# Kernel tuning notes

Measured on AMD Instinct MI355X. Metric: run time of the kernel, lower is better.

## Reference

```python
import jax, jax.numpy as jnp
import numpy as np

SEQ, BATCH, HID = 4096, 32, 512


def setup_inputs() -> dict:
    key = jax.random.key(0)
    ks = jax.random.split(key, 7)
    s = 1.0 / np.sqrt(HID)
    return {
        "x0": jax.random.normal(ks[0], (SEQ, BATCH, 1), dtype=jnp.float32),
        "W_ih": jax.random.uniform(ks[1], (4 * HID, 1), jnp.float32, -s, s),
        "W_hh": jax.random.uniform(ks[2], (4 * HID, HID), jnp.float32, -s, s),
        "b_ih": jax.random.uniform(ks[3], (4 * HID,), jnp.float32, -s, s),
        "b_hh": jax.random.uniform(ks[4], (4 * HID,), jnp.float32, -s, s),
        "W_lin": jax.random.uniform(ks[5], (1, HID), jnp.float32, -s, s),
        "b_lin": jax.random.uniform(ks[6], (1,), jnp.float32, -s, s),
    }


def _lstm(x0, W_ih, W_hh, b_ih, b_hh):
    # x0: (T, B, 1). Precompute input contribution to gates for all steps.
    x_proj = jnp.einsum("tbi,gi->tbg", x0, W_ih) + (b_ih + b_hh)  # (T, B, 4H)
    T, B, _ = x_proj.shape
    H = W_hh.shape[1]
    h0 = jnp.zeros((B, H), x0.dtype)
    c0 = jnp.zeros((B, H), x0.dtype)

    def step(carry, xp):
        h, c = carry
        gates = xp + h @ W_hh.T  # (B, 4H)
        i, f, g, o = jnp.split(gates, 4, axis=-1)  # torch gate order i,f,g,o
        i = jax.nn.sigmoid(i)
        f = jax.nn.sigmoid(f)
        g = jnp.tanh(g)
        o = jax.nn.sigmoid(o)
        c = f * c + i * g
        h = o * jnp.tanh(c)
        return (h, c), h

    _, hs = jax.lax.scan(step, (h0, c0), x_proj)  # hs: (T, B, H)
    return hs


def reference(x0, W_ih, W_hh, b_ih, b_hh, W_lin, b_lin):
    hs = _lstm(x0, W_ih, W_hh, b_ih, b_hh)            # (T, B, H)
    y = jnp.einsum("tbh,oh->tbo", hs, W_lin) + b_lin  # (T, B, 1)
    return y + x0                                      # residual add
```

## Files before the change

kernel.cpp:

```cpp
#include <hip/hip_runtime.h>
#include <stdint.h>

#define T_STEPS 4096
#define BATCH 32
#define HID 512
#define GROUPS 8
#define BLK_THREADS 1024

typedef _Float16 h2_t __attribute__((ext_vector_type(2)));

__device__ inline uint32_t pack_h2(float a, float b) {
  h2_t v;
  v.x = (_Float16)a;
  v.y = (_Float16)b;
  return __builtin_bit_cast(uint32_t, v);
}

__device__ inline float fdot2(uint32_t a, uint32_t b, float c) {
  return __builtin_amdgcn_fdot2(__builtin_bit_cast(h2_t, a),
                                __builtin_bit_cast(h2_t, b), c, false);
}

__device__ inline uint32_t aread(uint32_t a) {
  uint32_t v;
  asm("v_accvgpr_read_b32 %0, %1" : "=v"(v) : "a"(a));
  return v;
}

__device__ inline float sigf(float x) {
  return 1.0f / (1.0f + __expf(-x));
}
__device__ inline float tanh_fast(float x) {
  float a = fabsf(x);
  float e = __expf(-2.0f * a);
  float r = (1.0f - e) / (1.0f + e);
  return copysignf(r, x);
}

__global__ __launch_bounds__(BLK_THREADS, 4)
void lstm_persistent(const float* __restrict__ x0,
                     const float* __restrict__ W_ih,
                     const float* __restrict__ W_hh,
                     const float* __restrict__ b_ih,
                     const float* __restrict__ b_hh,
                     const float* __restrict__ W_lin,
                     const float* __restrict__ b_lin,
                     float* __restrict__ y,
                     uint32_t* __restrict__ h_ex)
{
  __shared__ float x0_lds[T_STEPS];
  __shared__ uint32_t trans[16][32];
  __shared__ float gacc[2][256];

  const int tid = threadIdx.x;
  const int xcd = blockIdx.x & 7;
  const int s   = blockIdx.x >> 3;
  const int g   = s & 7;
  const int b   = xcd + 8 * (s >> 3);
  const int u0  = g * 64;
  const int wv  = tid >> 6;
  const int rg  = wv >> 3;
  const int cs  = wv & 7;
  const int l   = tid & 63;

  uint32_t a0[32], a1[32];
  {
    const int r0 = 128 * rg + l;
    const int r1 = r0 + 64;
    const int R0 = (r0 >> 6) * HID + u0 + (r0 & 63);
    const int R1 = (r1 >> 6) * HID + u0 + (r1 & 63);
    const float2* p0 = (const float2*)(W_hh + (size_t)R0 * HID + 64 * cs);
    const float2* p1 = (const float2*)(W_hh + (size_t)R1 * HID + 64 * cs);
#pragma unroll
    for (int k = 0; k < 32; ++k) {
      float2 a = p0[k], c = p1[k];
      uint32_t t0 = pack_h2(a.x, a.y);
      uint32_t t1 = pack_h2(c.x, c.y);
      asm("v_accvgpr_write_b32 %0, %1" : "=a"(a0[k]) : "v"(t0));
      asm("v_accvgpr_write_b32 %0, %1" : "=a"(a1[k]) : "v"(t1));
    }
  }
  for (int i = tid; i < T_STEPS; i += BLK_THREADS) x0_lds[i] = x0[i * BATCH + b];
  if (tid < 256) { gacc[0][tid] = 0.f; gacc[1][tid] = 0.f; }

  float c_state = 0.f;
  float wih[4] = {0.f, 0.f, 0.f, 0.f}, bsum[4] = {0.f, 0.f, 0.f, 0.f};
  float wlin_u = 0.f, blin = 0.f;
  if (tid < 64) {
#pragma unroll
    for (int j = 0; j < 4; ++j) {
      int R = j * HID + u0 + tid;
      wih[j] = W_ih[R];
      bsum[j] = b_ih[R] + b_hh[R];
    }
    wlin_u = W_lin[u0 + tid];
    blin = b_lin[0];
  }
  __syncthreads();

  for (int t = 0; t < T_STEPS; ++t) {
    const int sl = t & 1, ns = sl ^ 1;

    const uint32_t* src =
        h_ex + ((size_t)sl * BATCH + b) * 512 + 64 * cs + l;
    uint32_t v;
    {
      const uint32_t tag = (uint32_t)t;
      int guard = 0;
      for (;;) {
        v = __hip_atomic_load(src, __ATOMIC_RELAXED,
                              __HIP_MEMORY_SCOPE_AGENT);
        if (__all((int)((v >> 16) == tag))) break;
        if (++guard > (1 << 20)) break;
        __builtin_amdgcn_s_sleep(1);
      }
    }

    if (l < 16) gacc[ns][wv * 16 + l] = 0.f;

    {
      uint32_t nv = __shfl_down(v, 1, 64);
      if ((l & 1) == 0) trans[wv][l >> 1] = (v & 0xffffu) | (nv << 16);
    }
    float acc0 = 0.f, acc1 = 0.f;
    const uint4* hp = (const uint4*)trans[wv];
#pragma unroll
    for (int q = 0; q < 8; ++q) {
      uint4 h4 = hp[q];
      const int k = 4 * q;
      acc0 = fdot2(aread(a0[k + 0]), h4.x, acc0); acc1 = fdot2(aread(a1[k + 0]), h4.x, acc1);
      acc0 = fdot2(aread(a0[k + 1]), h4.y, acc0); acc1 = fdot2(aread(a1[k + 1]), h4.y, acc1);
      acc0 = fdot2(aread(a0[k + 2]), h4.z, acc0); acc1 = fdot2(aread(a1[k + 2]), h4.z, acc1);
      acc0 = fdot2(aread(a0[k + 3]), h4.w, acc0); acc1 = fdot2(aread(a1[k + 3]), h4.w, acc1);
    }
    atomicAdd(&gacc[sl][128 * rg + l], acc0);
    atomicAdd(&gacc[sl][128 * rg + 64 + l], acc1);
    __syncthreads();

    if (tid < 64) {
      const float xv = x0_lds[t];
      float gi = gacc[sl][tid]       + xv * wih[0] + bsum[0];
      float gf = gacc[sl][tid + 64]  + xv * wih[1] + bsum[1];
      float gg = gacc[sl][tid + 128] + xv * wih[2] + bsum[2];
      float go = gacc[sl][tid + 192] + xv * wih[3] + bsum[3];
      float si = sigf(gi), sf = sigf(gf), tg = tanh_fast(gg), so = sigf(go);
      c_state = sf * c_state + si * tg;
      float h = so * tanh_fast(c_state);

      uint16_t hb = __builtin_bit_cast(uint16_t, (_Float16)h);
      uint32_t tagged = ((uint32_t)(t + 1) << 16) | (uint32_t)hb;
      uint32_t* dst = h_ex + ((size_t)ns * BATCH + b) * 512 + u0 + tid;
      __hip_atomic_store(dst, tagged, __ATOMIC_RELAXED,
                         __HIP_MEMORY_SCOPE_AGENT);

      float p = wlin_u * h;
#pragma unroll
      for (int m = 32; m >= 1; m >>= 1) p += __shfl_xor(p, m, 64);
      if (tid == 0) {
        if (g == 0) p += blin + xv;
        unsafeAtomicAdd(&y[t * BATCH + b], p);
      }
    }
  }
}

extern "C" void kernel_launch(void* const* d_in, const int* in_sizes, int n_in,
                              void* d_out, int out_size, void* d_ws, size_t ws_size,
                              hipStream_t stream) {
  const float* x0    = (const float*)d_in[0];
  const float* W_ih  = (const float*)d_in[1];
  const float* W_hh  = (const float*)d_in[2];
  const float* b_ih  = (const float*)d_in[3];
  const float* b_hh  = (const float*)d_in[4];
  const float* W_lin = (const float*)d_in[5];
  const float* b_lin = (const float*)d_in[6];
  float* y = (float*)d_out;

  uint32_t* h_ex = (uint32_t*)d_ws;
  const size_t init_bytes = 2 * BATCH * 512 * sizeof(uint32_t);

  hipMemsetAsync(d_ws, 0, init_bytes, stream);
  hipMemsetAsync(d_out, 0, (size_t)out_size * sizeof(float), stream);

  hipLaunchKernelGGL(lstm_persistent, dim3(BATCH * GROUPS), dim3(BLK_THREADS),
                     0, stream,
                     x0, W_ih, W_hh, b_ih, b_hh, W_lin, b_lin, y, h_ex);
}
```

Measured before the change: 16.81 ms.

## Map LSTM batch groups to XCDs dynamically and exchange hidden state via L2

Each block reads its hardware XCC ID and claims a slot through a per-XCD atomic counter, so that all 8 blocks cooperating on one batch element sit on the same XCD and share its L2. The hidden-state exchange now uses inline-asm global loads and stores with sc0 instead of agent-scope atomics, the spin loop drops s_sleep, and a sticky dead flag stops further polling once a timeout hits. Per-step output atomics to global memory are replaced by an LDS buffer that is flushed once at the end. This relies on the undocumented XCC_ID register and on the round-robin block placement holding 32 blocks per XCD; if the assumption fails, blocks exit early and the results are wrong.

```diff
diff --git a/kernel.cpp b/kernel.cpp
--- a/kernel.cpp
+++ b/kernel.cpp
@@ -6,6 +6,7 @@
 #define HID 512
 #define GROUPS 8
 #define BLK_THREADS 1024
+#define NBLOCKS 256
 
 typedef _Float16 h2_t __attribute__((ext_vector_type(2)));
 
@@ -27,9 +28,18 @@
   return v;
 }
 
-__device__ inline float sigf(float x) {
-  return 1.0f / (1.0f + __expf(-x));
-}
+__device__ inline uint32_t l2_load(const uint32_t* p) {
+  uint32_t v;
+  asm volatile("global_load_dword %0, %1, off sc0\n\ts_waitcnt vmcnt(0)"
+               : "=v"(v) : "v"(p) : "memory");
+  return v;
+}
+__device__ inline void l2_store(uint32_t* p, uint32_t v) {
+  asm volatile("global_store_dword %0, %1, off sc0" :: "v"(p), "v"(v)
+               : "memory");
+}
+
+__device__ inline float sigf(float x) { return 1.0f / (1.0f + __expf(-x)); }
 __device__ inline float tanh_fast(float x) {
   float a = fabsf(x);
   float e = __expf(-2.0f * a);
@@ -37,31 +47,43 @@
   return copysignf(r, x);
 }
 
-__global__ __launch_bounds__(BLK_THREADS, 4)
-void lstm_persistent(const float* __restrict__ x0,
-                     const float* __restrict__ W_ih,
-                     const float* __restrict__ W_hh,
-                     const float* __restrict__ b_ih,
-                     const float* __restrict__ b_hh,
-                     const float* __restrict__ W_lin,
-                     const float* __restrict__ b_lin,
-                     float* __restrict__ y,
-                     uint32_t* __restrict__ h_ex)
+__global__ __launch_bounds__(BLK_THREADS)
+void lstm_xcd(const float* __restrict__ x0,
+              const float* __restrict__ W_ih,
+              const float* __restrict__ W_hh,
+              const float* __restrict__ b_ih,
+              const float* __restrict__ b_hh,
+              const float* __restrict__ W_lin,
+              const float* __restrict__ b_lin,
+              float* __restrict__ y,
+              uint32_t* __restrict__ h_ex,
+              int* __restrict__ claim)
 {
   __shared__ float x0_lds[T_STEPS];
+  __shared__ float ylds[T_STEPS];
   __shared__ uint32_t trans[16][32];
   __shared__ float gacc[2][256];
+  __shared__ int s_bg;
 
   const int tid = threadIdx.x;
-  const int xcd = blockIdx.x & 7;
-  const int s   = blockIdx.x >> 3;
-  const int g   = s & 7;
-  const int b   = xcd + 8 * (s >> 3);
-  const int u0  = g * 64;
-  const int wv  = tid >> 6;
-  const int rg  = wv >> 3;
-  const int cs  = wv & 7;
-  const int l   = tid & 63;
+
+  if (tid == 0) {
+    uint32_t xcc;
+    asm volatile("s_getreg_b32 %0, hwreg(HW_REG_XCC_ID)" : "=s"(xcc));
+    xcc &= 7;
+    int slot = atomicAdd(claim + xcc * 16, 1);
+    s_bg = (slot < 32) ? (int)(((4 * xcc + (slot >> 3)) << 3) | (slot & 7))
+                       : -1;
+  }
+  __syncthreads();
+  if (s_bg < 0) return;
+  const int b  = s_bg >> 3;
+  const int g  = s_bg & 7;
+  const int u0 = g * 64;
+  const int wv = tid >> 6;
+  const int rg = wv >> 3;
+  const int cs = wv & 7;
+  const int l  = tid & 63;
 
   uint32_t a0[32], a1[32];
   {
@@ -80,39 +102,44 @@
       asm("v_accvgpr_write_b32 %0, %1" : "=a"(a1[k]) : "v"(t1));
     }
   }
-  for (int i = tid; i < T_STEPS; i += BLK_THREADS) x0_lds[i] = x0[i * BATCH + b];
+  for (int i = tid; i < T_STEPS; i += BLK_THREADS) {
+    x0_lds[i] = x0[i * BATCH + b];
+    ylds[i] = 0.f;
+  }
   if (tid < 256) { gacc[0][tid] = 0.f; gacc[1][tid] = 0.f; }
 
   float c_state = 0.f;
-  float wih[4] = {0.f, 0.f, 0.f, 0.f}, bsum[4] = {0.f, 0.f, 0.f, 0.f};
+  float wih_[4] = {0.f, 0.f, 0.f, 0.f}, bs_[4] = {0.f, 0.f, 0.f, 0.f};
   float wlin_u = 0.f, blin = 0.f;
   if (tid < 64) {
 #pragma unroll
     for (int j = 0; j < 4; ++j) {
       int R = j * HID + u0 + tid;
-      wih[j] = W_ih[R];
-      bsum[j] = b_ih[R] + b_hh[R];
+      wih_[j] = W_ih[R];
+      bs_[j] = b_ih[R] + b_hh[R];
     }
     wlin_u = W_lin[u0 + tid];
     blin = b_lin[0];
   }
+
+  uint32_t* hb = h_ex + (size_t)b * 1024;
+  const uint32_t* src01[2] = { hb + 64 * cs + l, hb + 512 + 64 * cs + l };
+  uint32_t* dst01[2] = { hb + u0 + tid, hb + 512 + u0 + tid };
+
   __syncthreads();
 
+  int dead = 0;
   for (int t = 0; t < T_STEPS; ++t) {
     const int sl = t & 1, ns = sl ^ 1;
 
-    const uint32_t* src =
-        h_ex + ((size_t)sl * BATCH + b) * 512 + 64 * cs + l;
     uint32_t v;
     {
-      const uint32_t tag = (uint32_t)t;
+      const uint32_t* sp = src01[sl];
       int guard = 0;
       for (;;) {
-        v = __hip_atomic_load(src, __ATOMIC_RELAXED,
-                              __HIP_MEMORY_SCOPE_AGENT);
-        if (__all((int)((v >> 16) == tag))) break;
-        if (++guard > (1 << 20)) break;
-        __builtin_amdgcn_s_sleep(1);
+        v = l2_load(sp);
+        if (__all((int)((v >> 16) == (uint32_t)t))) break;
+        if (dead || ++guard > (1 << 17)) { dead = 1; break; }
       }
     }
 
@@ -139,28 +166,29 @@
 
     if (tid < 64) {
       const float xv = x0_lds[t];
-      float gi = gacc[sl][tid]       + xv * wih[0] + bsum[0];
-      float gf = gacc[sl][tid + 64]  + xv * wih[1] + bsum[1];
-      float gg = gacc[sl][tid + 128] + xv * wih[2] + bsum[2];
-      float go = gacc[sl][tid + 192] + xv * wih[3] + bsum[3];
-      float si = sigf(gi), sf = sigf(gf), tg = tanh_fast(gg), so = sigf(go);
-      c_state = sf * c_state + si * tg;
+      float gi = gacc[sl][tid]       + xv * wih_[0] + bs_[0];
+      float gf = gacc[sl][tid + 64]  + xv * wih_[1] + bs_[1];
+      float gg = gacc[sl][tid + 128] + xv * wih_[2] + bs_[2];
+      float go = gacc[sl][tid + 192] + xv * wih_[3] + bs_[3];
+      float si = sigf(gi), sf = sigf(gf), tg_ = tanh_fast(gg), so = sigf(go);
+      c_state = sf * c_state + si * tg_;
       float h = so * tanh_fast(c_state);
 
-      uint16_t hb = __builtin_bit_cast(uint16_t, (_Float16)h);
-      uint32_t tagged = ((uint32_t)(t + 1) << 16) | (uint32_t)hb;
-      uint32_t* dst = h_ex + ((size_t)ns * BATCH + b) * 512 + u0 + tid;
-      __hip_atomic_store(dst, tagged, __ATOMIC_RELAXED,
-                         __HIP_MEMORY_SCOPE_AGENT);
+      uint16_t hbb = __builtin_bit_cast(uint16_t, (_Float16)h);
+      l2_store(dst01[ns], ((uint32_t)(t + 1) << 16) | (uint32_t)hbb);
 
       float p = wlin_u * h;
 #pragma unroll
       for (int m = 32; m >= 1; m >>= 1) p += __shfl_xor(p, m, 64);
-      if (tid == 0) {
-        if (g == 0) p += blin + xv;
-        unsafeAtomicAdd(&y[t * BATCH + b], p);
-      }
-    }
+      if (tid == 0) ylds[t] = p;
+    }
+  }
+
+  __syncthreads();
+  for (int i = tid; i < T_STEPS; i += BLK_THREADS) {
+    float val = ylds[i];
+    if (g == 0) val += blin + x0_lds[i];
+    unsafeAtomicAdd(&y[i * BATCH + b], val);
   }
 }
 
@@ -177,12 +205,13 @@
   float* y = (float*)d_out;
 
   uint32_t* h_ex = (uint32_t*)d_ws;
-  const size_t init_bytes = 2 * BATCH * 512 * sizeof(uint32_t);
+  int* claim = (int*)((char*)d_ws + (size_t)BATCH * 1024 * sizeof(uint32_t));
+  const size_t init_bytes =
+      (size_t)BATCH * 1024 * sizeof(uint32_t) + 8 * 16 * sizeof(int);
 
   hipMemsetAsync(d_ws, 0, init_bytes, stream);
   hipMemsetAsync(d_out, 0, (size_t)out_size * sizeof(float), stream);
 
-  hipLaunchKernelGGL(lstm_persistent, dim3(BATCH * GROUPS), dim3(BLK_THREADS),
-                     0, stream,
-                     x0, W_ih, W_hh, b_ih, b_hh, W_lin, b_lin, y, h_ex);
-}
+  hipLaunchKernelGGL(lstm_xcd, dim3(NBLOCKS), dim3(BLK_THREADS), 0, stream,
+                     x0, W_ih, W_hh, b_ih, b_hh, W_lin, b_lin, y, h_ex, claim);
+}
```

Result: slower. 28.46 ms (+69.3%).
